# Kernel optimization log

Measured on AMD Instinct MI355X. Metric: run time of the kernel, lower is better.

The kernel has to match this reference:

```python
import jax, jax.numpy as jnp
import numpy as np

D_MODEL = 1024
N_HEADS = 16
D_HEAD = D_MODEL // N_HEADS
D_FF = 4096
EPS = 1e-6  # flax LayerNorm default


def setup_inputs() -> dict:
    key = jax.random.key(0)
    ks = jax.random.split(key, 16)
    s = 1.0 / np.sqrt(D_MODEL)
    inp = {
        'x':  jax.random.normal(ks[0], (4, 2048, D_MODEL), jnp.float32),
        'Wq': jax.random.normal(ks[1], (D_MODEL, D_MODEL), jnp.float32) * s,
        'bq': jnp.zeros((D_MODEL,), jnp.float32),
        'Wk': jax.random.normal(ks[2], (D_MODEL, D_MODEL), jnp.float32) * s,
        'bk': jnp.zeros((D_MODEL,), jnp.float32),
        'Wv': jax.random.normal(ks[3], (D_MODEL, D_MODEL), jnp.float32) * s,
        'bv': jnp.zeros((D_MODEL,), jnp.float32),
        'Wo': jax.random.normal(ks[4], (D_MODEL, D_MODEL), jnp.float32) * s,
        'W1': jax.random.normal(ks[5], (D_MODEL, D_FF), jnp.float32) * s,
        'b1': jnp.zeros((D_FF,), jnp.float32),
        'W2': jax.random.normal(ks[6], (D_FF, D_MODEL), jnp.float32) * (1.0 / np.sqrt(D_FF)),
        'b2': jnp.zeros((D_MODEL,), jnp.float32),
        'g1': jnp.ones((D_MODEL,), jnp.float32),
        'beta1': jnp.zeros((D_MODEL,), jnp.float32),
        'g2': jnp.ones((D_MODEL,), jnp.float32),
        'beta2': jnp.zeros((D_MODEL,), jnp.float32),
    }
    return inp


def _layernorm(x, g, b):
    mu = jnp.mean(x, axis=-1, keepdims=True)
    var = jnp.mean(jnp.square(x - mu), axis=-1, keepdims=True)
    return (x - mu) * jax.lax.rsqrt(var + EPS) * g + b


def _attention(x, Wq, bq, Wk, bk, Wv, bv, Wo):
    B, S, D = x.shape
    def split_heads(t):
        return t.reshape(B, S, N_HEADS, D_HEAD).transpose(0, 2, 1, 3)  # bhsd
    q = split_heads(x @ Wq + bq)
    k = split_heads(x @ Wk + bk)
    v = split_heads(x @ Wv + bv)
    scale = jnp.sqrt(jnp.float32(D_HEAD))
    scores = jnp.einsum('bhsd,bhtd->bhst', q, k) / scale
    causal = jnp.tril(jnp.ones((S, S), dtype=jnp.bool_))
    scores = jnp.where(causal, scores, jnp.finfo(scores.dtype).min)
    w = jax.nn.softmax(scores, axis=-1)
    out = jnp.einsum('bhst,bhtd->bhsd', w, v)
    out = out.transpose(0, 2, 1, 3).reshape(B, S, D)
    return out @ Wo  # o_proj has no bias


def reference(x, Wq, bq, Wk, bk, Wv, bv, Wo, W1, b1, W2, b2, g1, beta1, g2, beta2):
    normed = _layernorm(x, g1, beta1)
    x = x + _attention(normed, Wq, bq, Wk, bk, Wv, bv, Wo)
    normed = _layernorm(x, g2, beta2)
    h = jax.nn.gelu(normed @ W1 + b1)  # approximate tanh gelu, matching flax nn.gelu
    x = x + (h @ W2 + b2)
    return x
```

## Files before the change

### kernel.cpp

```cpp
#include <hip/hip_runtime.h>

#define SEQ 2048
#define NROWS 8192
#define NH 16
#define DHEAD 64
#define QLD 3072

typedef float f32x4 __attribute__((ext_vector_type(4)));
typedef __bf16 bf16x8 __attribute__((ext_vector_type(8)));

__device__ __forceinline__ unsigned short f2bf(float f) {
  union { float f; unsigned u; } v; v.f = f;
  unsigned r = v.u + 0x7fffu + ((v.u >> 16) & 1u);
  return (unsigned short)(r >> 16);
}

__device__ __forceinline__ void gl16(const void* g, void* l) {
  __builtin_amdgcn_global_load_lds((const __attribute__((address_space(1))) void*)g,
                                   (__attribute__((address_space(3))) void*)l, 16, 0, 0);
}

__device__ __forceinline__ float gelu_f(float x) {
  float t = 0.7978845608028654f * (x + 0.044715f * x * x * x);
  float e = __expf(2.0f * t);
  float th = 1.0f - 2.0f / (e + 1.0f);
  return 0.5f * x * (1.0f + th);
}

#define CVTPK(dst, lo, hi) asm("v_cvt_pk_bf16_f32 %0, %1, %2" : "=v"(dst) : "v"(lo), "v"(hi))

#if __has_builtin(__builtin_amdgcn_permlane32_swap)
#define P32SWAP(a, b, x, y) { auto _t = __builtin_amdgcn_permlane32_swap((a), (b), false, false); (x) = _t[0]; (y) = _t[1]; }
#else
#define P32SWAP(a, b, x, y) { unsigned _as = (unsigned)__shfl_xor((int)(a), 32, 64); \
  unsigned _bs = (unsigned)__shfl_xor((int)(b), 32, 64); \
  (x) = (l < 32) ? (a) : _bs; (y) = (l < 32) ? _as : (b); }
#endif
#if __has_builtin(__builtin_amdgcn_permlane16_swap)
#define P16SWAP(a, b, x, y) { auto _t = __builtin_amdgcn_permlane16_swap((a), (b), false, false); (x) = _t[0]; (y) = _t[1]; }
#else
#define P16SWAP(a, b, x, y) { unsigned _as = (unsigned)__shfl_xor((int)(a), 16, 64); \
  unsigned _bs = (unsigned)__shfl_xor((int)(b), 16, 64); \
  (x) = (l & 16) ? _bs : (a); (y) = (l & 16) ? (b) : _as; }
#endif

#define MEMFENCE asm volatile("" ::: "memory")
#define BAR() do { MEMFENCE; __builtin_amdgcn_s_barrier(); MEMFENCE; } while (0)
#define WAIT_LGKM0 asm volatile("s_waitcnt lgkmcnt(0)" ::: "memory")
#define WAIT_VM0 asm volatile("s_waitcnt vmcnt(0)" ::: "memory")

__global__ __launch_bounds__(256) void transpose_cvt(const float* __restrict__ W,
                                                     unsigned short* __restrict__ Wt,
                                                     int K, int N) {
  __shared__ float tile[32][33];
  const int tx = threadIdx.x, ty = threadIdx.y;
  const int n0 = blockIdx.x * 32, k0 = blockIdx.y * 32;
#pragma unroll
  for (int i = ty; i < 32; i += 8)
    tile[i][tx] = W[(size_t)(k0 + i) * N + n0 + tx];
  __syncthreads();
#pragma unroll
  for (int i = ty; i < 32; i += 8)
    Wt[(size_t)(n0 + i) * K + k0 + tx] = f2bf(tile[tx][i]);
}

__global__ __launch_bounds__(256) void concat_bias(const float* __restrict__ bq,
                                                   const float* __restrict__ bk,
                                                   const float* __restrict__ bv,
                                                   float* __restrict__ dst) {
  int i = blockIdx.x * 256 + threadIdx.x;
  if (i < 1024) dst[i] = bq[i];
  else if (i < 2048) dst[i] = bk[i - 1024];
  else if (i < 3072) dst[i] = bv[i - 2048];
}

__global__ __launch_bounds__(256) void layernorm_k(const float* __restrict__ x,
                                                   const float* __restrict__ g,
                                                   const float* __restrict__ b,
                                                   unsigned short* __restrict__ out) {
  const int row = blockIdx.x, tid = threadIdx.x;
  const float4 v = reinterpret_cast<const float4*>(x + (size_t)row * 1024)[tid];
  float s = v.x + v.y + v.z + v.w;
  float s2 = v.x * v.x + v.y * v.y + v.z * v.z + v.w * v.w;
#pragma unroll
  for (int d = 1; d < 64; d <<= 1) { s += __shfl_xor(s, d, 64); s2 += __shfl_xor(s2, d, 64); }
  __shared__ float ls[4], ls2[4];
  const int w = tid >> 6;
  if ((tid & 63) == 0) { ls[w] = s; ls2[w] = s2; }
  __syncthreads();
  s = ls[0] + ls[1] + ls[2] + ls[3];
  s2 = ls2[0] + ls2[1] + ls2[2] + ls2[3];
  const float mu = s * (1.0f / 1024.0f);
  const float var = s2 * (1.0f / 1024.0f) - mu * mu;
  const float rstd = rsqrtf(var + 1e-6f);
  const float4 gv = reinterpret_cast<const float4*>(g)[tid];
  const float4 bv = reinterpret_cast<const float4*>(b)[tid];
  ushort4 o;
  o.x = f2bf((v.x - mu) * rstd * gv.x + bv.x);
  o.y = f2bf((v.y - mu) * rstd * gv.y + bv.y);
  o.z = f2bf((v.z - mu) * rstd * gv.z + bv.z);
  o.w = f2bf((v.w - mu) * rstd * gv.w + bv.w);
  reinterpret_cast<ushort4*>(out + (size_t)row * 1024)[tid] = o;
}

enum { EP_BIAS = 1, EP_RES = 2, EP_GELU = 4, EP_BF16 = 8, EP_QSCALE = 16 };

template <int BN, int E>
__global__ __launch_bounds__(512, 2) void gemm8_k(const unsigned short* __restrict__ A,
                                                  const unsigned short* __restrict__ Bt,
                                                  const float* __restrict__ bias,
                                                  const float* __restrict__ resid,
                                                  void* __restrict__ out,
                                                  int M, int N, int K) {
  constexpr int BM = 256;
  constexpr int NWC = (BN == 256) ? 4 : 2;
  constexpr int WM = (BN == 256) ? 128 : 64;
  constexpr int MI = WM / 16;
  constexpr int MQ = MI / 2;
  __shared__ __align__(16) unsigned short As[2][BM * 64];
  __shared__ __align__(16) unsigned short Bs[2][BN * 64];

  const int tid = threadIdx.x;
  const int l = tid & 63, w = tid >> 6;
  const int lr = l & 15, lg = l >> 4;
  const int wr = w / NWC, wc = w % NWC;

  const int gx = gridDim.x;
  const int nwg = gx * gridDim.y;
  int lin = blockIdx.y * gx + blockIdx.x;
  lin = (lin & 7) * (nwg >> 3) + (lin >> 3);
  const int bn = lin % gx, bm = lin / gx;

  const unsigned short* Ab = A + (size_t)(bm * BM) * K;
  const unsigned short* Bb = Bt + (size_t)(bn * BN) * K;

  const int srow = l >> 3;
  const int sslot = (l & 7) ^ (srow & 7);
  auto stA = [&](int buf, int t, int seg) {
    gl16((const char*)(Ab + (size_t)(seg * 8 + srow) * K + t * 64) + sslot * 16,
         (char*)As[buf] + seg * 1024 + l * 16);
  };
  auto stB = [&](int buf, int t, int seg) {
    gl16((const char*)(Bb + (size_t)(seg * 8 + srow) * K + t * 64) + sslot * 16,
         (char*)Bs[buf] + seg * 1024 + l * 16);
  };
  auto stage = [&](int buf, int t, int p) {
    if (BN == 256) {
      if (p == 0)      { stA(buf, t, w); stA(buf, t, 8 + w);  stB(buf, t, w); }
      else if (p == 1) { stA(buf, t, 16 + w); stA(buf, t, 24 + w); stB(buf, t, 8 + w); }
      else if (p == 2) { stB(buf, t, 16 + w); stB(buf, t, 24 + w); }
    } else {
      if (p == 0)      { stA(buf, t, w); stB(buf, t, w); }
      else if (p == 1) { stA(buf, t, 8 + w); stB(buf, t, 8 + w); }
      else if (p == 2) { stA(buf, t, 16 + w); stA(buf, t, 24 + w); }
    }
  };
  auto rdA = [&](int buf, int r, int ks) {
    return *reinterpret_cast<const bf16x8*>(
        (const char*)As[buf] + r * 128 + (((ks << 2) + lg) ^ (r & 7)) * 16);
  };
  auto rdB = [&](int buf, int r, int ks) {
    return *reinterpret_cast<const bf16x8*>(
        (const char*)Bs[buf] + r * 128 + (((ks << 2) + lg) ^ (r & 7)) * 16);
  };

  f32x4 acc[MI][4];
#pragma unroll
  for (int m = 0; m < MI; ++m)
#pragma unroll
    for (int n = 0; n < 4; ++n) acc[m][n] = 0.0f;

  const int NK = K >> 6;
#pragma unroll
  for (int p = 0; p < 3; ++p) stage(0, 0, p);
  WAIT_VM0;
  BAR();

#pragma unroll 2
  for (int kt = 0; kt < NK; ++kt) {
    const int c = kt & 1, nb = c ^ 1;
    const bool more = kt + 1 < NK;
    bf16x8 a0[MQ][2], a1[MQ][2], b0[2][2], b1[2][2];

#pragma unroll
    for (int mi = 0; mi < MQ; ++mi)
#pragma unroll
      for (int ks = 0; ks < 2; ++ks) a0[mi][ks] = rdA(c, wr * WM + mi * 16 + lr, ks);
#pragma unroll
    for (int ni = 0; ni < 2; ++ni)
#pragma unroll
      for (int ks = 0; ks < 2; ++ks) b0[ni][ks] = rdB(c, wc * 64 + ni * 16 + lr, ks);
    if (more) stage(nb, kt + 1, 0);
    BAR();
    WAIT_LGKM0;
    __builtin_amdgcn_s_setprio(1);
#pragma unroll
    for (int mi = 0; mi < MQ; ++mi)
#pragma unroll
      for (int ni = 0; ni < 2; ++ni)
#pragma unroll
        for (int ks = 0; ks < 2; ++ks)
          acc[mi][ni] = __builtin_amdgcn_mfma_f32_16x16x32_bf16(a0[mi][ks], b0[ni][ks], acc[mi][ni], 0, 0, 0);
    __builtin_amdgcn_s_setprio(0);
    BAR();

#pragma unroll
    for (int ni = 0; ni < 2; ++ni)
#pragma unroll
      for (int ks = 0; ks < 2; ++ks) b1[ni][ks] = rdB(c, wc * 64 + (2 + ni) * 16 + lr, ks);
    if (more) stage(nb, kt + 1, 1);
    BAR();
    WAIT_LGKM0;
    __builtin_amdgcn_s_setprio(1);
#pragma unroll
    for (int mi = 0; mi < MQ; ++mi)
#pragma unroll
      for (int ni = 0; ni < 2; ++ni)
#pragma unroll
        for (int ks = 0; ks < 2; ++ks)
          acc[mi][2 + ni] = __builtin_amdgcn_mfma_f32_16x16x32_bf16(a0[mi][ks], b1[ni][ks], acc[mi][2 + ni], 0, 0, 0);
    __builtin_amdgcn_s_setprio(0);
    BAR();

#pragma unroll
    for (int mi = 0; mi < MQ; ++mi)
#pragma unroll
      for (int ks = 0; ks < 2; ++ks) a1[mi][ks] = rdA(c, wr * WM + (MQ + mi) * 16 + lr, ks);
    if (more) stage(nb, kt + 1, 2);
    BAR();
    WAIT_LGKM0;
    __builtin_amdgcn_s_setprio(1);
#pragma unroll
    for (int mi = 0; mi < MQ; ++mi)
#pragma unroll
      for (int ni = 0; ni < 2; ++ni)
#pragma unroll
        for (int ks = 0; ks < 2; ++ks)
          acc[MQ + mi][ni] = __builtin_amdgcn_mfma_f32_16x16x32_bf16(a1[mi][ks], b0[ni][ks], acc[MQ + mi][ni], 0, 0, 0);
    __builtin_amdgcn_s_setprio(0);
    BAR();

    __builtin_amdgcn_s_setprio(1);
#pragma unroll
    for (int mi = 0; mi < MQ; ++mi)
#pragma unroll
      for (int ni = 0; ni < 2; ++ni)
#pragma unroll
        for (int ks = 0; ks < 2; ++ks)
          acc[MQ + mi][2 + ni] = __builtin_amdgcn_mfma_f32_16x16x32_bf16(a1[mi][ks], b1[ni][ks], acc[MQ + mi][2 + ni], 0, 0, 0);
    __builtin_amdgcn_s_setprio(0);
    WAIT_VM0;
    BAR();
  }

  const int row0 = bm * BM + wr * WM;
  const int col0 = bn * BN + wc * 64;
#pragma unroll
  for (int m = 0; m < MI; ++m) {
#pragma unroll
    for (int n = 0; n < 4; ++n) {
      const int col = col0 + n * 16 + lr;
      float bc = 0.0f;
      if (E & EP_BIAS) bc = bias[col];
#pragma unroll
      for (int j = 0; j < 4; ++j) {
        const int row = row0 + m * 16 + lg * 4 + j;
        float v = acc[m][n][j] + bc;
        if (E & EP_RES) v += resid[(size_t)row * N + col];
        if (E & EP_GELU) v = gelu_f(v);
        if (E & EP_QSCALE) { if (col < 1024) v *= 0.125f; }
        if (E & EP_BF16) ((unsigned short*)out)[(size_t)row * N + col] = f2bf(v);
        else ((float*)out)[(size_t)row * N + col] = v;
      }
    }
  }
}

__global__ __launch_bounds__(512, 4) void attn_k(const unsigned short* __restrict__ qkv,
                                                 unsigned short* __restrict__ out) {
  __shared__ __align__(16) unsigned short Kl[2][4096];
  __shared__ __align__(16) unsigned short Vt[2][4096];
  const int tid = threadIdx.x;
  const int l = tid & 63, w = tid >> 6;
  const int lr = l & 15, lg = l >> 4;
  const int bh = blockIdx.y;
  const int b = bh >> 4, h = bh & 15;
  const size_t rowbase = (size_t)b * SEQ;
  char* klb = (char*)Kl;
  char* vtb = (char*)Vt;
  const int sg = tid & 15, dhg = tid >> 4;

  auto stageK = [&](int buf, int kb2) {
    const int r = (w << 3) + (l >> 3);
    const char* src = (const char*)(qkv + (rowbase + kb2 + r) * QLD + 1024 + h * 64)
                      + 16 * ((l & 7) ^ (l >> 3));
    gl16(src, klb + buf * 8192 + (w << 10) + (l << 4));
  };
  auto loadV = [&](int kb2, uint2* vr) {
    if (tid < 256) {
#pragma unroll
      for (int i = 0; i < 4; ++i)
        vr[i] = *reinterpret_cast<const uint2*>(
            qkv + (rowbase + kb2 + sg * 4 + i) * QLD + 2048 + h * 64 + dhg * 4);
    }
  };
  auto writeV = [&](int buf, const uint2* vr) {
    if (tid < 256) {
      char* vb = vtb + buf * 8192;
#pragma unroll
      for (int jj = 0; jj < 4; ++jj) {
        const int dh = dhg * 4 + jj;
        unsigned a0 = (jj < 2) ? vr[0].x : vr[0].y;
        unsigned a1 = (jj < 2) ? vr[1].x : vr[1].y;
        unsigned a2 = (jj < 2) ? vr[2].x : vr[2].y;
        unsigned a3 = (jj < 2) ? vr[3].x : vr[3].y;
        unsigned s01, s23;
        if (jj & 1) {
          s01 = (a0 >> 16) | (a1 & 0xffff0000u);
          s23 = (a2 >> 16) | (a3 & 0xffff0000u);
        } else {
          s01 = (a0 & 0xffffu) | (a1 << 16);
          s23 = (a2 & 0xffffu) | (a3 << 16);
        }
        const int bo = (dh * 128 + sg * 8) ^ ((dh & 7) << 4);
        uint2 p; p.x = s01; p.y = s23;
        *reinterpret_cast<uint2*>(vb + bo) = p;
      }
    }
  };

#pragma unroll 1
  for (int seg = 0; seg < 2; ++seg) {
    const int qt = seg ? (15 - blockIdx.x) : blockIdx.x;
    const int q0 = qt << 7;
    const int ktmax = 2 * qt + 1;
    const int qwmin = q0 + w * 16;
    const int qrow = qwmin + lr;

    bf16x8 qf[2];
#pragma unroll
    for (int ks = 0; ks < 2; ++ks)
      qf[ks] = *reinterpret_cast<const bf16x8*>(
          qkv + (rowbase + qrow) * QLD + h * 64 + ks * 32 + lg * 8);

    f32x4 oacc[4];
#pragma unroll
    for (int n = 0; n < 4; ++n) oacc[n] = 0.0f;
    float mrun = -1e30f, lrun = 0.0f;

    {
      stageK(0, 0);
      uint2 vr[4];
      loadV(0, vr);
      writeV(0, vr);
    }
    __syncthreads();

#pragma unroll 1
    for (int kt = 0; kt <= ktmax; ++kt) {
      const int cur = kt & 1, nb = cur ^ 1;
      const int kb = kt << 6;
      const bool more = kt < ktmax;
      const bool active = kb <= qwmin + 15;
      uint2 vr[4];
      if (more) { stageK(nb, (kt + 1) << 6); loadV((kt + 1) << 6, vr); }

      f32x4 sacc[4];
      if (active) {
#pragma unroll
        for (int ni = 0; ni < 4; ++ni) sacc[ni] = 0.0f;
        const char* kc = klb + cur * 8192;
        __builtin_amdgcn_s_setprio(1);
#pragma unroll
        for (int ks = 0; ks < 2; ++ks) {
#pragma unroll
          for (int ni = 0; ni < 4; ++ni) {
            const int r = ni * 16 + lr;
            const int bo = (r * 128 + ks * 64 + lg * 16) ^ ((lr & 7) << 4);
            bf16x8 kf = *reinterpret_cast<const bf16x8*>(kc + bo);
            sacc[ni] = __builtin_amdgcn_mfma_f32_16x16x32_bf16(kf, qf[ks], sacc[ni], 0, 0, 0);
          }
        }
        __builtin_amdgcn_s_setprio(0);

        if (kb + 63 > qwmin) {
#pragma unroll
          for (int ni = 0; ni < 4; ++ni)
#pragma unroll
            for (int j = 0; j < 4; ++j)
              if (kb + ni * 16 + lg * 4 + j > qrow) sacc[ni][j] = -1e30f;
        }

        float pm = sacc[0][0];
#pragma unroll
        for (int ni = 0; ni < 4; ++ni)
#pragma unroll
          for (int j = 0; j < 4; ++j) pm = fmaxf(pm, sacc[ni][j]);
        pm = fmaxf(pm, __shfl_xor(pm, 16, 64));
        pm = fmaxf(pm, __shfl_xor(pm, 32, 64));
        const float mnew = fmaxf(mrun, pm);
        const float alpha = __expf(mrun - mnew);
        mrun = mnew;
        float rs = 0.0f;
#pragma unroll
        for (int ni = 0; ni < 4; ++ni)
#pragma unroll
          for (int j = 0; j < 4; ++j) {
            const float p = __expf(sacc[ni][j] - mnew);
            sacc[ni][j] = p;
            rs += p;
          }
        rs += __shfl_xor(rs, 16, 64);
        rs += __shfl_xor(rs, 32, 64);
        lrun = lrun * alpha + rs;
#pragma unroll
        for (int n = 0; n < 4; ++n) oacc[n] *= alpha;
      }

      if (more) writeV(nb, vr);

      if (active) {
        const char* vc = vtb + cur * 8192;
#pragma unroll
        for (int ks2 = 0; ks2 < 2; ++ks2) {
          unsigned U0, U1, U2, U3, C0, C1, W0, W1, W2, W3;
          CVTPK(U0, sacc[2 * ks2][0], sacc[2 * ks2][1]);
          CVTPK(U1, sacc[2 * ks2][2], sacc[2 * ks2][3]);
          CVTPK(U2, sacc[2 * ks2 + 1][0], sacc[2 * ks2 + 1][1]);
          CVTPK(U3, sacc[2 * ks2 + 1][2], sacc[2 * ks2 + 1][3]);
          P32SWAP(U0, U2, C0, C1);
          P16SWAP(C0, C1, W0, W2);
          P32SWAP(U1, U3, C0, C1);
          P16SWAP(C0, C1, W1, W3);
          union { uint4 u; bf16x8 v; } pu;
          pu.u = make_uint4(W0, W1, W2, W3);
          __builtin_amdgcn_s_setprio(1);
#pragma unroll
          for (int n = 0; n < 4; ++n) {
            const int r = n * 16 + lr;
            const int bo = (r * 128 + ks2 * 64 + lg * 16) ^ ((lr & 7) << 4);
            bf16x8 vf = *reinterpret_cast<const bf16x8*>(vc + bo);
            oacc[n] = __builtin_amdgcn_mfma_f32_16x16x32_bf16(vf, pu.v, oacc[n], 0, 0, 0);
          }
          __builtin_amdgcn_s_setprio(0);
        }
      }
      __syncthreads();
    }

    const float inv = 1.0f / lrun;
#pragma unroll
    for (int n = 0; n < 4; ++n) {
      ushort4 o;
      o.x = f2bf(oacc[n][0] * inv);
      o.y = f2bf(oacc[n][1] * inv);
      o.z = f2bf(oacc[n][2] * inv);
      o.w = f2bf(oacc[n][3] * inv);
      *reinterpret_cast<ushort4*>(out + (rowbase + qrow) * 1024 + h * 64 + n * 16 + lg * 4) = o;
    }
  }
}

extern "C" void kernel_launch(void* const* d_in, const int* in_sizes, int n_in,
                              void* d_out, int out_size, void* d_ws, size_t ws_size,
                              hipStream_t stream) {
  const float* x   = (const float*)d_in[0];
  const float* Wq  = (const float*)d_in[1];
  const float* bq  = (const float*)d_in[2];
  const float* Wk  = (const float*)d_in[3];
  const float* bk  = (const float*)d_in[4];
  const float* Wv  = (const float*)d_in[5];
  const float* bv  = (const float*)d_in[6];
  const float* Wo  = (const float*)d_in[7];
  const float* W1  = (const float*)d_in[8];
  const float* b1  = (const float*)d_in[9];
  const float* W2  = (const float*)d_in[10];
  const float* b2  = (const float*)d_in[11];
  const float* g1  = (const float*)d_in[12];
  const float* be1 = (const float*)d_in[13];
  const float* g2  = (const float*)d_in[14];
  const float* be2 = (const float*)d_in[15];

  char* ws = (char*)d_ws;
  size_t off = 0;
  auto alloc = [&](size_t bytes) { char* p = ws + off; off += (bytes + 255) & ~(size_t)255; return p; };
  unsigned short* WqkvT = (unsigned short*)alloc((size_t)3072 * 1024 * 2);
  unsigned short* WoT   = (unsigned short*)alloc((size_t)1024 * 1024 * 2);
  unsigned short* W1T   = (unsigned short*)alloc((size_t)4096 * 1024 * 2);
  unsigned short* W2T   = (unsigned short*)alloc((size_t)1024 * 4096 * 2);
  float*          bqkv  = (float*)alloc((size_t)3072 * 4);
  unsigned short* normed = (unsigned short*)alloc((size_t)NROWS * 1024 * 2);
  unsigned short* qkvbuf = (unsigned short*)alloc((size_t)NROWS * 4096 * 2);
  unsigned short* attnb  = (unsigned short*)alloc((size_t)NROWS * 1024 * 2);
  float*          x1     = (float*)alloc((size_t)NROWS * 1024 * 4);

  const dim3 tb(32, 8);
  transpose_cvt<<<dim3(32, 32), tb, 0, stream>>>(Wq, WqkvT, 1024, 1024);
  transpose_cvt<<<dim3(32, 32), tb, 0, stream>>>(Wk, WqkvT + 1024 * 1024, 1024, 1024);
  transpose_cvt<<<dim3(32, 32), tb, 0, stream>>>(Wv, WqkvT + 2 * 1024 * 1024, 1024, 1024);
  transpose_cvt<<<dim3(32, 32), tb, 0, stream>>>(Wo, WoT, 1024, 1024);
  transpose_cvt<<<dim3(128, 32), tb, 0, stream>>>(W1, W1T, 1024, 4096);
  transpose_cvt<<<dim3(32, 128), tb, 0, stream>>>(W2, W2T, 4096, 1024);
  concat_bias<<<12, 256, 0, stream>>>(bq, bk, bv, bqkv);

  layernorm_k<<<NROWS, 256, 0, stream>>>(x, g1, be1, normed);
  gemm8_k<256, (EP_BIAS | EP_BF16 | EP_QSCALE)><<<dim3(12, 32), 512, 0, stream>>>(normed, WqkvT, bqkv, nullptr, qkvbuf, NROWS, 3072, 1024);
  attn_k<<<dim3(8, 64), 512, 0, stream>>>(qkvbuf, attnb);
  gemm8_k<128, EP_RES><<<dim3(8, 32), 512, 0, stream>>>(attnb, WoT, nullptr, x, x1, NROWS, 1024, 1024);
  layernorm_k<<<NROWS, 256, 0, stream>>>(x1, g2, be2, normed);
  gemm8_k<256, (EP_BIAS | EP_GELU | EP_BF16)><<<dim3(16, 32), 512, 0, stream>>>(normed, W1T, b1, nullptr, qkvbuf, NROWS, 4096, 1024);
  gemm8_k<128, (EP_BIAS | EP_RES)><<<dim3(8, 32), 512, 0, stream>>>(qkvbuf, W2T, b2, x1, d_out, NROWS, 1024, 4096);
}
```

Baseline: 535.6 us.

## Widen attention KV tiles, use exp2 softmax with lazy rescale, retile narrow GEMMs

Attention now processes 128-key tiles per step with a wider swizzled transposed-V layout. All 512 threads load V, and the per-warp activity gating is dropped. Softmax moves to exp2 by folding log2(e) into the Q scale, and the output rescale is skipped unless the running max grows by more than a threshold. The GEMM template is re-parameterised to a fixed 256-wide N tile with variable M tile, the narrow GEMMs are relaunched as 128x256 tiles, and each k-step's full tile is staged up front instead of in three phases. Risks are extra wasted work on diagonal tiles, more LDS use lowering occupancy, and less overlap between loads and compute in the GEMMs.

```diff
diff --git a/kernel.cpp b/kernel.cpp
--- a/kernel.cpp
+++ b/kernel.cpp
@@ -105,16 +105,15 @@
 
 enum { EP_BIAS = 1, EP_RES = 2, EP_GELU = 4, EP_BF16 = 8, EP_QSCALE = 16 };
 
-template <int BN, int E>
+template <int BM, int E>
 __global__ __launch_bounds__(512, 2) void gemm8_k(const unsigned short* __restrict__ A,
                                                   const unsigned short* __restrict__ Bt,
                                                   const float* __restrict__ bias,
                                                   const float* __restrict__ resid,
                                                   void* __restrict__ out,
                                                   int M, int N, int K) {
-  constexpr int BM = 256;
-  constexpr int NWC = (BN == 256) ? 4 : 2;
-  constexpr int WM = (BN == 256) ? 128 : 64;
+  constexpr int BN = 256;
+  constexpr int WM = BM / 2;
   constexpr int MI = WM / 16;
   constexpr int MQ = MI / 2;
   __shared__ __align__(16) unsigned short As[2][BM * 64];
@@ -123,7 +122,7 @@
   const int tid = threadIdx.x;
   const int l = tid & 63, w = tid >> 6;
   const int lr = l & 15, lg = l >> 4;
-  const int wr = w / NWC, wc = w % NWC;
+  const int wr = w >> 2, wc = w & 3;
 
   const int gx = gridDim.x;
   const int nwg = gx * gridDim.y;
@@ -134,34 +133,28 @@
   const unsigned short* Ab = A + (size_t)(bm * BM) * K;
   const unsigned short* Bb = Bt + (size_t)(bn * BN) * K;
 
-  const int srow = l >> 3;
-  const int sslot = (l & 7) ^ (srow & 7);
-  auto stA = [&](int buf, int t, int seg) {
-    gl16((const char*)(Ab + (size_t)(seg * 8 + srow) * K + t * 64) + sslot * 16,
-         (char*)As[buf] + seg * 1024 + l * 16);
-  };
-  auto stB = [&](int buf, int t, int seg) {
-    gl16((const char*)(Bb + (size_t)(seg * 8 + srow) * K + t * 64) + sslot * 16,
-         (char*)Bs[buf] + seg * 1024 + l * 16);
-  };
-  auto stage = [&](int buf, int t, int p) {
-    if (BN == 256) {
-      if (p == 0)      { stA(buf, t, w); stA(buf, t, 8 + w);  stB(buf, t, w); }
-      else if (p == 1) { stA(buf, t, 16 + w); stA(buf, t, 24 + w); stB(buf, t, 8 + w); }
-      else if (p == 2) { stB(buf, t, 16 + w); stB(buf, t, 24 + w); }
-    } else {
-      if (p == 0)      { stA(buf, t, w); stB(buf, t, w); }
-      else if (p == 1) { stA(buf, t, 8 + w); stB(buf, t, 8 + w); }
-      else if (p == 2) { stA(buf, t, 16 + w); stA(buf, t, 24 + w); }
-    }
+  const int srow8 = l >> 3;
+  const int slot = (l & 7) ^ (srow8 & 7);
+  auto stA = [&](int buf, int t, int s) {
+    gl16((const char*)(Ab + (size_t)(s * 8 + srow8) * K + t * 64) + slot * 16,
+         (char*)(&As[buf][0]) + s * 1024 + l * 16);
+  };
+  auto stB = [&](int buf, int t, int s) {
+    gl16((const char*)(Bb + (size_t)(s * 8 + srow8) * K + t * 64) + slot * 16,
+         (char*)(&Bs[buf][0]) + s * 1024 + l * 16);
+  };
+  auto stageAll = [&](int buf, int t) {
+    stA(buf, t, w); stA(buf, t, 8 + w);
+    if (BM == 256) { stA(buf, t, 16 + w); stA(buf, t, 24 + w); }
+    stB(buf, t, w); stB(buf, t, 8 + w); stB(buf, t, 16 + w); stB(buf, t, 24 + w);
   };
   auto rdA = [&](int buf, int r, int ks) {
     return *reinterpret_cast<const bf16x8*>(
-        (const char*)As[buf] + r * 128 + (((ks << 2) + lg) ^ (r & 7)) * 16);
+        (const char*)(&As[buf][0]) + r * 128 + (((ks << 2) + lg) ^ (r & 7)) * 16);
   };
   auto rdB = [&](int buf, int r, int ks) {
     return *reinterpret_cast<const bf16x8*>(
-        (const char*)Bs[buf] + r * 128 + (((ks << 2) + lg) ^ (r & 7)) * 16);
+        (const char*)(&Bs[buf][0]) + r * 128 + (((ks << 2) + lg) ^ (r & 7)) * 16);
   };
 
   f32x4 acc[MI][4];
@@ -171,8 +164,7 @@
     for (int n = 0; n < 4; ++n) acc[m][n] = 0.0f;
 
   const int NK = K >> 6;
-#pragma unroll
-  for (int p = 0; p < 3; ++p) stage(0, 0, p);
+  stageAll(0, 0);
   WAIT_VM0;
   BAR();
 
@@ -182,6 +174,7 @@
     const bool more = kt + 1 < NK;
     bf16x8 a0[MQ][2], a1[MQ][2], b0[2][2], b1[2][2];
 
+    if (more) stageAll(nb, kt + 1);
 #pragma unroll
     for (int mi = 0; mi < MQ; ++mi)
 #pragma unroll
@@ -190,7 +183,6 @@
     for (int ni = 0; ni < 2; ++ni)
 #pragma unroll
       for (int ks = 0; ks < 2; ++ks) b0[ni][ks] = rdB(c, wc * 64 + ni * 16 + lr, ks);
-    if (more) stage(nb, kt + 1, 0);
     BAR();
     WAIT_LGKM0;
     __builtin_amdgcn_s_setprio(1);
@@ -208,7 +200,6 @@
     for (int ni = 0; ni < 2; ++ni)
 #pragma unroll
       for (int ks = 0; ks < 2; ++ks) b1[ni][ks] = rdB(c, wc * 64 + (2 + ni) * 16 + lr, ks);
-    if (more) stage(nb, kt + 1, 1);
     BAR();
     WAIT_LGKM0;
     __builtin_amdgcn_s_setprio(1);
@@ -226,7 +217,6 @@
     for (int mi = 0; mi < MQ; ++mi)
 #pragma unroll
       for (int ks = 0; ks < 2; ++ks) a1[mi][ks] = rdA(c, wr * WM + (MQ + mi) * 16 + lr, ks);
-    if (more) stage(nb, kt + 1, 2);
     BAR();
     WAIT_LGKM0;
     __builtin_amdgcn_s_setprio(1);
@@ -268,7 +258,7 @@
         float v = acc[m][n][j] + bc;
         if (E & EP_RES) v += resid[(size_t)row * N + col];
         if (E & EP_GELU) v = gelu_f(v);
-        if (E & EP_QSCALE) { if (col < 1024) v *= 0.125f; }
+        if (E & EP_QSCALE) { if (col < 1024) v *= 0.18033688011112042f; }
         if (E & EP_BF16) ((unsigned short*)out)[(size_t)row * N + col] = f2bf(v);
         else ((float*)out)[(size_t)row * N + col] = v;
       }
@@ -278,8 +268,8 @@
 
 __global__ __launch_bounds__(512, 4) void attn_k(const unsigned short* __restrict__ qkv,
                                                  unsigned short* __restrict__ out) {
-  __shared__ __align__(16) unsigned short Kl[2][4096];
-  __shared__ __align__(16) unsigned short Vt[2][4096];
+  __shared__ __align__(16) unsigned short Kl[2][128 * 64];
+  __shared__ __align__(16) unsigned short Vt[2][64 * 128];
   const int tid = threadIdx.x;
   const int l = tid & 63, w = tid >> 6;
   const int lr = l & 15, lg = l >> 4;
@@ -288,44 +278,44 @@
   const size_t rowbase = (size_t)b * SEQ;
   char* klb = (char*)Kl;
   char* vtb = (char*)Vt;
-  const int sg = tid & 15, dhg = tid >> 4;
-
+
+  const int srow8 = l >> 3;
+  const int kslot = (l & 7) ^ (srow8 & 7);
   auto stageK = [&](int buf, int kb2) {
-    const int r = (w << 3) + (l >> 3);
-    const char* src = (const char*)(qkv + (rowbase + kb2 + r) * QLD + 1024 + h * 64)
-                      + 16 * ((l & 7) ^ (l >> 3));
-    gl16(src, klb + buf * 8192 + (w << 10) + (l << 4));
-  };
+#pragma unroll
+    for (int s = w; s < 16; s += 8) {
+      const char* src = (const char*)(qkv + (rowbase + kb2 + s * 8 + srow8) * QLD + 1024 + h * 64)
+                        + kslot * 16;
+      gl16(src, klb + buf * 16384 + s * 1024 + l * 16);
+    }
+  };
+  const int sg = tid & 31, dhg = tid >> 5;
   auto loadV = [&](int kb2, uint2* vr) {
-    if (tid < 256) {
-#pragma unroll
-      for (int i = 0; i < 4; ++i)
-        vr[i] = *reinterpret_cast<const uint2*>(
-            qkv + (rowbase + kb2 + sg * 4 + i) * QLD + 2048 + h * 64 + dhg * 4);
-    }
+#pragma unroll
+    for (int i = 0; i < 4; ++i)
+      vr[i] = *reinterpret_cast<const uint2*>(
+          qkv + (rowbase + kb2 + sg * 4 + i) * QLD + 2048 + h * 64 + dhg * 4);
   };
   auto writeV = [&](int buf, const uint2* vr) {
-    if (tid < 256) {
-      char* vb = vtb + buf * 8192;
-#pragma unroll
-      for (int jj = 0; jj < 4; ++jj) {
-        const int dh = dhg * 4 + jj;
-        unsigned a0 = (jj < 2) ? vr[0].x : vr[0].y;
-        unsigned a1 = (jj < 2) ? vr[1].x : vr[1].y;
-        unsigned a2 = (jj < 2) ? vr[2].x : vr[2].y;
-        unsigned a3 = (jj < 2) ? vr[3].x : vr[3].y;
-        unsigned s01, s23;
-        if (jj & 1) {
-          s01 = (a0 >> 16) | (a1 & 0xffff0000u);
-          s23 = (a2 >> 16) | (a3 & 0xffff0000u);
-        } else {
-          s01 = (a0 & 0xffffu) | (a1 << 16);
-          s23 = (a2 & 0xffffu) | (a3 << 16);
-        }
-        const int bo = (dh * 128 + sg * 8) ^ ((dh & 7) << 4);
-        uint2 p; p.x = s01; p.y = s23;
-        *reinterpret_cast<uint2*>(vb + bo) = p;
+    char* vb = vtb + buf * 16384;
+#pragma unroll
+    for (int jj = 0; jj < 4; ++jj) {
+      const int dh = dhg * 4 + jj;
+      unsigned a0 = (jj < 2) ? vr[0].x : vr[0].y;
+      unsigned a1 = (jj < 2) ? vr[1].x : vr[1].y;
+      unsigned a2 = (jj < 2) ? vr[2].x : vr[2].y;
+      unsigned a3 = (jj < 2) ? vr[3].x : vr[3].y;
+      unsigned s01, s23;
+      if (jj & 1) {
+        s01 = (a0 >> 16) | (a1 & 0xffff0000u);
+        s23 = (a2 >> 16) | (a3 & 0xffff0000u);
+      } else {
+        s01 = (a0 & 0xffffu) | (a1 << 16);
+        s23 = (a2 & 0xffffu) | (a3 << 16);
       }
+      const int bo = dh * 256 + (((sg >> 1) ^ (dh & 15)) << 4) + ((sg & 1) << 3);
+      uint2 p; p.x = s01; p.y = s23;
+      *reinterpret_cast<uint2*>(vb + bo) = p;
     }
   };
 
@@ -333,7 +323,6 @@
   for (int seg = 0; seg < 2; ++seg) {
     const int qt = seg ? (15 - blockIdx.x) : blockIdx.x;
     const int q0 = qt << 7;
-    const int ktmax = 2 * qt + 1;
     const int qwmin = q0 + w * 16;
     const int qrow = qwmin + lr;
 
@@ -350,100 +339,98 @@
 
     {
       stageK(0, 0);
-      uint2 vr[4];
-      loadV(0, vr);
-      writeV(0, vr);
+      uint2 vr0[4];
+      loadV(0, vr0);
+      writeV(0, vr0);
     }
     __syncthreads();
 
 #pragma unroll 1
-    for (int kt = 0; kt <= ktmax; ++kt) {
+    for (int kt = 0; kt <= qt; ++kt) {
       const int cur = kt & 1, nb = cur ^ 1;
-      const int kb = kt << 6;
-      const bool more = kt < ktmax;
-      const bool active = kb <= qwmin + 15;
+      const int kb = kt << 7;
+      const bool more = kt < qt;
       uint2 vr[4];
-      if (more) { stageK(nb, (kt + 1) << 6); loadV((kt + 1) << 6, vr); }
-
-      f32x4 sacc[4];
-      if (active) {
-#pragma unroll
-        for (int ni = 0; ni < 4; ++ni) sacc[ni] = 0.0f;
-        const char* kc = klb + cur * 8192;
+      if (more) { stageK(nb, kb + 128); loadV(kb + 128, vr); }
+
+      f32x4 sacc[8];
+#pragma unroll
+      for (int ni = 0; ni < 8; ++ni) sacc[ni] = 0.0f;
+      const char* kc = klb + cur * 16384;
+      __builtin_amdgcn_s_setprio(1);
+#pragma unroll
+      for (int ks = 0; ks < 2; ++ks) {
+#pragma unroll
+        for (int ni = 0; ni < 8; ++ni) {
+          const int r = ni * 16 + lr;
+          const int bo = r * 128 + ((((ks << 2) + lg) ^ (r & 7)) << 4);
+          bf16x8 kf = *reinterpret_cast<const bf16x8*>(kc + bo);
+          sacc[ni] = __builtin_amdgcn_mfma_f32_16x16x32_bf16(kf, qf[ks], sacc[ni], 0, 0, 0);
+        }
+      }
+      __builtin_amdgcn_s_setprio(0);
+
+      if (kt == qt) {
+#pragma unroll
+        for (int ni = 0; ni < 8; ++ni)
+#pragma unroll
+          for (int j = 0; j < 4; ++j)
+            if (kb + ni * 16 + lg * 4 + j > qrow) sacc[ni][j] = -1e30f;
+      }
+
+      float pm = sacc[0][0];
+#pragma unroll
+      for (int ni = 0; ni < 8; ++ni)
+#pragma unroll
+        for (int j = 0; j < 4; ++j) pm = fmaxf(pm, sacc[ni][j]);
+      pm = fmaxf(pm, __shfl_xor(pm, 16, 64));
+      pm = fmaxf(pm, __shfl_xor(pm, 32, 64));
+      if (!__all(pm <= mrun + 8.0f)) {
+        const float mnew = fmaxf(mrun, pm);
+        const float alpha = exp2f(mrun - mnew);
+        mrun = mnew;
+        lrun *= alpha;
+#pragma unroll
+        for (int n = 0; n < 4; ++n) oacc[n] *= alpha;
+      }
+      float rs = 0.0f;
+#pragma unroll
+      for (int ni = 0; ni < 8; ++ni)
+#pragma unroll
+        for (int j = 0; j < 4; ++j) {
+          const float p = exp2f(sacc[ni][j] - mrun);
+          sacc[ni][j] = p;
+          rs += p;
+        }
+      rs += __shfl_xor(rs, 16, 64);
+      rs += __shfl_xor(rs, 32, 64);
+      lrun += rs;
+
+      if (more) writeV(nb, vr);
+
+      const char* vc = vtb + cur * 16384;
+#pragma unroll
+      for (int g = 0; g < 4; ++g) {
+        unsigned U0, U1, U2, U3, C0, C1, W0, W1, W2, W3;
+        CVTPK(U0, sacc[2 * g][0], sacc[2 * g][1]);
+        CVTPK(U1, sacc[2 * g][2], sacc[2 * g][3]);
+        CVTPK(U2, sacc[2 * g + 1][0], sacc[2 * g + 1][1]);
+        CVTPK(U3, sacc[2 * g + 1][2], sacc[2 * g + 1][3]);
+        P32SWAP(U0, U2, C0, C1);
+        P16SWAP(C0, C1, W0, W2);
+        P32SWAP(U1, U3, C0, C1);
+        P16SWAP(C0, C1, W1, W3);
+        union { uint4 u; bf16x8 v; } pu;
+        pu.u = make_uint4(W0, W1, W2, W3);
         __builtin_amdgcn_s_setprio(1);
 #pragma unroll
-        for (int ks = 0; ks < 2; ++ks) {
-#pragma unroll
-          for (int ni = 0; ni < 4; ++ni) {
-            const int r = ni * 16 + lr;
-            const int bo = (r * 128 + ks * 64 + lg * 16) ^ ((lr & 7) << 4);
-            bf16x8 kf = *reinterpret_cast<const bf16x8*>(kc + bo);
-            sacc[ni] = __builtin_amdgcn_mfma_f32_16x16x32_bf16(kf, qf[ks], sacc[ni], 0, 0, 0);
-          }
+        for (int n = 0; n < 4; ++n) {
+          const int r = n * 16 + lr;
+          const int bo = r * 256 + ((((g << 2) + lg) ^ (r & 15)) << 4);
+          bf16x8 vf = *reinterpret_cast<const bf16x8*>(vc + bo);
+          oacc[n] = __builtin_amdgcn_mfma_f32_16x16x32_bf16(vf, pu.v, oacc[n], 0, 0, 0);
         }
         __builtin_amdgcn_s_setprio(0);
-
-        if (kb + 63 > qwmin) {
-#pragma unroll
-          for (int ni = 0; ni < 4; ++ni)
-#pragma unroll
-            for (int j = 0; j < 4; ++j)
-              if (kb + ni * 16 + lg * 4 + j > qrow) sacc[ni][j] = -1e30f;
-        }
-
-        float pm = sacc[0][0];
-#pragma unroll
-        for (int ni = 0; ni < 4; ++ni)
-#pragma unroll
-          for (int j = 0; j < 4; ++j) pm = fmaxf(pm, sacc[ni][j]);
-        pm = fmaxf(pm, __shfl_xor(pm, 16, 64));
-        pm = fmaxf(pm, __shfl_xor(pm, 32, 64));
-        const float mnew = fmaxf(mrun, pm);
-        const float alpha = __expf(mrun - mnew);
-        mrun = mnew;
-        float rs = 0.0f;
-#pragma unroll
-        for (int ni = 0; ni < 4; ++ni)
-#pragma unroll
-          for (int j = 0; j < 4; ++j) {
-            const float p = __expf(sacc[ni][j] - mnew);
-            sacc[ni][j] = p;
-            rs += p;
-          }
-        rs += __shfl_xor(rs, 16, 64);
-        rs += __shfl_xor(rs, 32, 64);
-        lrun = lrun * alpha + rs;
-#pragma unroll
-        for (int n = 0; n < 4; ++n) oacc[n] *= alpha;
-      }
-
-      if (more) writeV(nb, vr);
-
-      if (active) {
-        const char* vc = vtb + cur * 8192;
-#pragma unroll
-        for (int ks2 = 0; ks2 < 2; ++ks2) {
-          unsigned U0, U1, U2, U3, C0, C1, W0, W1, W2, W3;
-          CVTPK(U0, sacc[2 * ks2][0], sacc[2 * ks2][1]);
-          CVTPK(U1, sacc[2 * ks2][2], sacc[2 * ks2][3]);
-          CVTPK(U2, sacc[2 * ks2 + 1][0], sacc[2 * ks2 + 1][1]);
-          CVTPK(U3, sacc[2 * ks2 + 1][2], sacc[2 * ks2 + 1][3]);
-          P32SWAP(U0, U2, C0, C1);
-          P16SWAP(C0, C1, W0, W2);
-          P32SWAP(U1, U3, C0, C1);
-          P16SWAP(C0, C1, W1, W3);
-          union { uint4 u; bf16x8 v; } pu;
-          pu.u = make_uint4(W0, W1, W2, W3);
-          __builtin_amdgcn_s_setprio(1);
-#pragma unroll
-          for (int n = 0; n < 4; ++n) {
-            const int r = n * 16 + lr;
-            const int bo = (r * 128 + ks2 * 64 + lg * 16) ^ ((lr & 7) << 4);
-            bf16x8 vf = *reinterpret_cast<const bf16x8*>(vc + bo);
-            oacc[n] = __builtin_amdgcn_mfma_f32_16x16x32_bf16(vf, pu.v, oacc[n], 0, 0, 0);
-          }
-          __builtin_amdgcn_s_setprio(0);
-        }
       }
       __syncthreads();
     }
@@ -506,8 +493,8 @@
   layernorm_k<<<NROWS, 256, 0, stream>>>(x, g1, be1, normed);
   gemm8_k<256, (EP_BIAS | EP_BF16 | EP_QSCALE)><<<dim3(12, 32), 512, 0, stream>>>(normed, WqkvT, bqkv, nullptr, qkvbuf, NROWS, 3072, 1024);
   attn_k<<<dim3(8, 64), 512, 0, stream>>>(qkvbuf, attnb);
-  gemm8_k<128, EP_RES><<<dim3(8, 32), 512, 0, stream>>>(attnb, WoT, nullptr, x, x1, NROWS, 1024, 1024);
+  gemm8_k<128, EP_RES><<<dim3(4, 64), 512, 0, stream>>>(attnb, WoT, nullptr, x, x1, NROWS, 1024, 1024);
   layernorm_k<<<NROWS, 256, 0, stream>>>(x1, g2, be2, normed);
   gemm8_k<256, (EP_BIAS | EP_GELU | EP_BF16)><<<dim3(16, 32), 512, 0, stream>>>(normed, W1T, b1, nullptr, qkvbuf, NROWS, 4096, 1024);
-  gemm8_k<128, (EP_BIAS | EP_RES)><<<dim3(8, 32), 512, 0, stream>>>(qkvbuf, W2T, b2, x1, d_out, NROWS, 1024, 4096);
-}
+  gemm8_k<128, (EP_BIAS | EP_RES)><<<dim3(4, 64), 512, 0, stream>>>(qkvbuf, W2T, b2, x1, d_out, NROWS, 1024, 4096);
+}
```

After: 596.0 us. 11.3% more time.
